# Kernel tuning notes

Hardware: AMD Instinct MI355X
Metric: run time of the kernel (lower is better)

## Reference

```python
import jax, jax.numpy as jnp
import numpy as np

N = 100000
E = 1600000
F_IN, F_HID, F_OUT = 128, 64, 1


def setup_inputs() -> dict:
    key = jax.random.key(0)
    ks = jax.random.split(key, 8)
    x = jax.random.normal(ks[0], (N, F_IN), dtype=jnp.float32)
    edge_index = jax.random.randint(ks[1], (2, E), 0, N, dtype=jnp.int64)
    def glorot(k, fan_in, fan_out):
        scale = jnp.sqrt(2.0 / (fan_in + fan_out)).astype(jnp.float32)
        return jax.random.normal(k, (fan_in, fan_out), dtype=jnp.float32) * scale
    W1 = glorot(ks[2], F_IN, F_HID); b1 = jnp.zeros((F_HID,), jnp.float32)
    W2 = glorot(ks[3], F_HID, F_HID); b2 = jnp.zeros((F_HID,), jnp.float32)
    W3 = glorot(ks[4], F_HID, F_OUT); b3 = jnp.zeros((F_OUT,), jnp.float32)
    return {"x": x, "W1": W1, "b1": b1, "W2": W2, "b2": b2, "W3": W3, "b3": b3, "edge_index": edge_index}


def _gcn_norm(edge_index, n):
    # add self-loops, symmetric D^{-1/2} (A+I) D^{-1/2} normalization (PyG GCNConv default)
    loop = jnp.arange(n, dtype=edge_index.dtype)
    src = jnp.concatenate([edge_index[0], loop])
    dst = jnp.concatenate([edge_index[1], loop])
    deg = jax.ops.segment_sum(jnp.ones_like(src, dtype=jnp.float32), dst, num_segments=n)
    dis = jnp.where(deg > 0, jax.lax.rsqrt(jnp.maximum(deg, 1.0)), 0.0)
    norm = dis[src] * dis[dst]  # [E+N]
    return src, dst, norm


def _gcn_conv(h, W, b, src, dst, norm, n):
    h = h @ W                                   # [N, f_out]
    msg = h[src] * norm[:, None]                # gather + scale, [E+N, f_out]
    out = jax.ops.segment_sum(msg, dst, num_segments=n)  # scatter-add
    return out + b


def reference(x, W1, b1, W2, b2, W3, b3, edge_index):
    n = x.shape[0]
    src, dst, norm = _gcn_norm(edge_index, n)
    h = jax.nn.relu(_gcn_conv(x, W1, b1, src, dst, norm, n))
    h = jax.nn.relu(_gcn_conv(h, W2, b2, src, dst, norm, n))
    h = _gcn_conv(h, W3, b3, src, dst, norm, n)
    return jax.nn.sigmoid(h)
```

## Files before the change

kernel.cpp:

```cpp
#include <hip/hip_runtime.h>
#include <math.h>

#define NN 100000
#define NE 1600000
#define NSHARD 4
#define SHARD_W (NN / NSHARD)
#define NCHUNK 64
#define CHUNK_E (NE / NCHUNK)
#define CHUNK_I4 (CHUNK_E / 4)

typedef __attribute__((ext_vector_type(8))) short bf16x8;
typedef __attribute__((ext_vector_type(4))) float f32x4;
typedef __attribute__((ext_vector_type(2))) float f32x2;

__device__ inline unsigned f2bf(float f) {
    unsigned u = __float_as_uint(f);
    u += 0x7FFFu + ((u >> 16) & 1u);
    return u >> 16;
}
__device__ inline float bflo(unsigned v) { return __uint_as_float(v << 16); }
__device__ inline float bfhi(unsigned v) { return __uint_as_float(v & 0xFFFF0000u); }
__device__ inline f32x2 bfpair(unsigned u) {
    f32x2 r;
    r.x = __uint_as_float(u << 16);
    r.y = __uint_as_float(u & 0xFFFF0000u);
    return r;
}

__global__ __launch_bounds__(256) void k_cnt(const int4* __restrict__ dst4,
                                             unsigned char* __restrict__ cnt,
                                             unsigned char* __restrict__ lrank) {
    __shared__ __align__(16) unsigned ldeg[SHARD_W];
    int t = threadIdx.x;
    int shard = blockIdx.x & (NSHARD - 1);
    int b = blockIdx.x >> 2;
    int lo = shard * SHARD_W;
    uint4 z4 = make_uint4(0u, 0u, 0u, 0u);
    for (int i = t; i < SHARD_W / 4; i += 256) ((uint4*)ldeg)[i] = z4;
    __syncthreads();
    const int4* p = dst4 + b * CHUNK_I4;
    unsigned char* lr = lrank + b * CHUNK_E;
#pragma unroll 4
    for (int j = t; j < CHUNK_I4; j += 256) {
        int4 d = p[j];
        unsigned ex = (unsigned)(d.x - lo);
        unsigned ey = (unsigned)(d.y - lo);
        unsigned ez = (unsigned)(d.z - lo);
        unsigned ew = (unsigned)(d.w - lo);
        if (ex < SHARD_W) lr[4 * j + 0] = (unsigned char)atomicAdd(&ldeg[ex], 1u);
        if (ey < SHARD_W) lr[4 * j + 1] = (unsigned char)atomicAdd(&ldeg[ey], 1u);
        if (ez < SHARD_W) lr[4 * j + 2] = (unsigned char)atomicAdd(&ldeg[ez], 1u);
        if (ew < SHARD_W) lr[4 * j + 3] = (unsigned char)atomicAdd(&ldeg[ew], 1u);
    }
    __syncthreads();
    unsigned* cb32 = (unsigned*)cnt + b * (NN / 4) + shard * (SHARD_W / 4);
    for (int i = t; i < SHARD_W / 4; i += 256) {
        uint4 v = *(const uint4*)&ldeg[4 * i];
        cb32[i] = (v.x & 255u) | ((v.y & 255u) << 8) | ((v.z & 255u) << 16)
                | ((v.w & 255u) << 24);
    }
}

__global__ __launch_bounds__(256) void k_blkscan(unsigned* __restrict__ cnt32,
                                                 int4* __restrict__ deg4) {
    int i = blockIdx.x * 256 + threadIdx.x;
    if (i >= NN / 4) return;
    unsigned c[NCHUNK];
#pragma unroll
    for (int b = 0; b < NCHUNK; ++b) c[b] = cnt32[b * (NN / 4) + i];
    unsigned a0 = 0, a1 = 0, a2 = 0, a3 = 0;
#pragma unroll
    for (int b = 0; b < NCHUNK; ++b) {
        unsigned v = c[b];
        cnt32[b * (NN / 4) + i] = a0 | (a1 << 8) | (a2 << 16) | (a3 << 24);
        a0 += v & 255u;
        a1 += (v >> 8) & 255u;
        a2 += (v >> 16) & 255u;
        a3 += v >> 24;
    }
    deg4[i] = make_int4((int)a0, (int)a1, (int)a2, (int)a3);
}

__global__ void k_bsum(const int* __restrict__ deg, int* __restrict__ bsums) {
    __shared__ int s[256];
    int t = threadIdx.x;
    int i = blockIdx.x * 256 + t;
    s[t] = (i < NN) ? deg[i] : 0;
    __syncthreads();
    for (int off = 128; off > 0; off >>= 1) {
        if (t < off) s[t] += s[t + off];
        __syncthreads();
    }
    if (t == 0) bsums[blockIdx.x] = s[0];
}

__global__ void k_scan512(const int* __restrict__ bsums, int* __restrict__ bscan) {
    __shared__ int s[512];
    int t = threadIdx.x;
    int v = (t < 391) ? bsums[t] : 0;
    s[t] = v;
    __syncthreads();
    for (int off = 1; off < 512; off <<= 1) {
        int x = (t >= off) ? s[t - off] : 0;
        __syncthreads();
        s[t] += x;
        __syncthreads();
    }
    bscan[t] = s[t] - v;
}

__global__ void k_rowptr(const int* __restrict__ deg, const int* __restrict__ bscan,
                         int* __restrict__ rowptr, float* __restrict__ dis) {
    __shared__ int s[256];
    int t = threadIdx.x;
    int i = blockIdx.x * 256 + t;
    int d = (i < NN) ? deg[i] : 0;
    s[t] = d;
    __syncthreads();
    for (int off = 1; off < 256; off <<= 1) {
        int x = (t >= off) ? s[t - off] : 0;
        __syncthreads();
        s[t] += x;
        __syncthreads();
    }
    if (i < NN) {
        int rp = bscan[blockIdx.x] + s[t] - d;
        rowptr[i] = rp;
        dis[i] = rsqrtf((float)(d + 1));
    }
    if (i == 0) rowptr[NN] = NE;
}

__global__ __launch_bounds__(256) void k_build_csr(
    const int4* __restrict__ src4, const int4* __restrict__ dst4,
    const unsigned char* __restrict__ blkoff, const unsigned* __restrict__ lr4,
    const int* __restrict__ rowptr, int* __restrict__ csr) {
    int shard = blockIdx.x & (NSHARD - 1);
    int bsh = blockIdx.x >> 2;
    int stride = (gridDim.x >> 2) * 256;
    int lo = shard * SHARD_W;
    const int NE4 = NE / 4;
    for (int i = bsh * 256 + threadIdx.x; i < NE4; i += stride) {
        int4 d = dst4[i];
        int4 s = src4[i];
        unsigned lr = lr4[i];
        const unsigned char* off = blkoff + (i / CHUNK_I4) * NN;
        unsigned ex = (unsigned)(d.x - lo);
        unsigned ey = (unsigned)(d.y - lo);
        unsigned ez = (unsigned)(d.z - lo);
        unsigned ew = (unsigned)(d.w - lo);
        if (ex < SHARD_W) csr[rowptr[d.x] + off[d.x] + (lr & 255u)] = s.x;
        if (ey < SHARD_W) csr[rowptr[d.y] + off[d.y] + ((lr >> 8) & 255u)] = s.y;
        if (ez < SHARD_W) csr[rowptr[d.z] + off[d.z] + ((lr >> 16) & 255u)] = s.z;
        if (ew < SHARD_W) csr[rowptr[d.w] + off[d.w] + (lr >> 24)] = s.w;
    }
}

#define XS_LD 136
__global__ __launch_bounds__(256) void k_gemm1(
    const float* __restrict__ x, const float* __restrict__ W,
    const float* __restrict__ dis, unsigned short* __restrict__ tsb) {
    __shared__ unsigned short xs[64 * XS_LD];
    __shared__ unsigned short wt[64 * XS_LD];
    int t = threadIdx.x;
    int row0 = blockIdx.x * 64;
    for (int i = t; i < 64 * 64; i += 256) {
        int n = i & 63, k2 = i >> 6;
        float w0 = W[(2 * k2) * 64 + n];
        float w1 = W[(2 * k2 + 1) * 64 + n];
        *(unsigned*)&wt[n * XS_LD + 2 * k2] = f2bf(w0) | (f2bf(w1) << 16);
    }
    for (int i = t; i < 64 * 32; i += 256) {
        int r = i >> 5, c4 = i & 31;
        int gr = row0 + r;
        uint2 p = {0u, 0u};
        if (gr < NN) {
            float4 v = *(const float4*)&x[gr * 128 + 4 * c4];
            p.x = f2bf(v.x) | (f2bf(v.y) << 16);
            p.y = f2bf(v.z) | (f2bf(v.w) << 16);
        }
        *(uint2*)&xs[r * XS_LD + 4 * c4] = p;
    }
    __syncthreads();
    int w = t >> 6, l = t & 63;
    int lm = l & 15, lg = l >> 4;
    const unsigned short* ap = &xs[(16 * w + lm) * XS_LD + 8 * lg];
    const unsigned short* bp = &wt[lm * XS_LD + 8 * lg];
    f32x4 acc0 = {0, 0, 0, 0}, acc1 = {0, 0, 0, 0}, acc2 = {0, 0, 0, 0}, acc3 = {0, 0, 0, 0};
#pragma unroll
    for (int kb = 0; kb < 4; ++kb) {
        bf16x8 a  = *(const bf16x8*)(ap + 32 * kb);
        bf16x8 b0 = *(const bf16x8*)(bp + 32 * kb);
        bf16x8 b1 = *(const bf16x8*)(bp + 16 * XS_LD + 32 * kb);
        bf16x8 b2 = *(const bf16x8*)(bp + 32 * XS_LD + 32 * kb);
        bf16x8 b3 = *(const bf16x8*)(bp + 48 * XS_LD + 32 * kb);
        acc0 = __builtin_amdgcn_mfma_f32_16x16x32_bf16(a, b0, acc0, 0, 0, 0);
        acc1 = __builtin_amdgcn_mfma_f32_16x16x32_bf16(a, b1, acc1, 0, 0, 0);
        acc2 = __builtin_amdgcn_mfma_f32_16x16x32_bf16(a, b2, acc2, 0, 0, 0);
        acc3 = __builtin_amdgcn_mfma_f32_16x16x32_bf16(a, b3, acc3, 0, 0, 0);
    }
    int rbase = row0 + 16 * w + 4 * lg;
#pragma unroll
    for (int r = 0; r < 4; ++r) {
        int row = rbase + r;
        if (row < NN) {
            float dv = dis[row];
            unsigned short* o = &tsb[row * 64 + lm];
            o[0]  = (unsigned short)f2bf(acc0[r] * dv);
            o[16] = (unsigned short)f2bf(acc1[r] * dv);
            o[32] = (unsigned short)f2bf(acc2[r] * dv);
            o[48] = (unsigned short)f2bf(acc3[r] * dv);
        }
    }
}

#define HS_LD 72
__global__ __launch_bounds__(256) void k_gemm2(
    const unsigned short* __restrict__ hb, const float* __restrict__ W,
    const float* __restrict__ dis, unsigned short* __restrict__ tsb) {
    __shared__ unsigned short hs[64 * HS_LD];
    __shared__ unsigned short wh[64 * HS_LD];
    __shared__ unsigned short wl[64 * HS_LD];
    int t = threadIdx.x;
    int row0 = blockIdx.x * 64;
    for (int i = t; i < 64 * 32; i += 256) {
        int n = i & 63, k2 = i >> 6;
        float w0 = W[(2 * k2) * 64 + n];
        float w1 = W[(2 * k2 + 1) * 64 + n];
        unsigned h0 = f2bf(w0), h1 = f2bf(w1);
        *(unsigned*)&wh[n * HS_LD + 2 * k2] = h0 | (h1 << 16);
        float r0 = w0 - bflo(h0), r1 = w1 - bflo(h1);
        *(unsigned*)&wl[n * HS_LD + 2 * k2] = f2bf(r0) | (f2bf(r1) << 16);
    }
    const uint4* h4 = (const uint4*)hb;
    for (int i = t; i < 64 * 8; i += 256) {
        int r = i >> 3, c8 = i & 7;
        int gr = row0 + r;
        uint4 v = (gr < NN) ? h4[gr * 8 + c8] : make_uint4(0u, 0u, 0u, 0u);
        *(uint4*)&hs[r * HS_LD + 8 * c8] = v;
    }
    __syncthreads();
    int w = t >> 6, l = t & 63;
    int lm = l & 15, lg = l >> 4;
    const unsigned short* ap = &hs[(16 * w + lm) * HS_LD + 8 * lg];
    const unsigned short* bh = &wh[lm * HS_LD + 8 * lg];
    const unsigned short* bl = &wl[lm * HS_LD + 8 * lg];
    f32x4 acc0 = {0, 0, 0, 0}, acc1 = {0, 0, 0, 0}, acc2 = {0, 0, 0, 0}, acc3 = {0, 0, 0, 0};
#pragma unroll
    for (int kb = 0; kb < 2; ++kb) {
        bf16x8 a  = *(const bf16x8*)(ap + 32 * kb);
        bf16x8 h0 = *(const bf16x8*)(bh + 32 * kb);
        bf16x8 h1 = *(const bf16x8*)(bh + 16 * HS_LD + 32 * kb);
        bf16x8 h2 = *(const bf16x8*)(bh + 32 * HS_LD + 32 * kb);
        bf16x8 h3 = *(const bf16x8*)(bh + 48 * HS_LD + 32 * kb);
        bf16x8 l0 = *(const bf16x8*)(bl + 32 * kb);
        bf16x8 l1 = *(const bf16x8*)(bl + 16 * HS_LD + 32 * kb);
        bf16x8 l2 = *(const bf16x8*)(bl + 32 * HS_LD + 32 * kb);
        bf16x8 l3 = *(const bf16x8*)(bl + 48 * HS_LD + 32 * kb);
        acc0 = __builtin_amdgcn_mfma_f32_16x16x32_bf16(a, h0, acc0, 0, 0, 0);
        acc1 = __builtin_amdgcn_mfma_f32_16x16x32_bf16(a, h1, acc1, 0, 0, 0);
        acc2 = __builtin_amdgcn_mfma_f32_16x16x32_bf16(a, h2, acc2, 0, 0, 0);
        acc3 = __builtin_amdgcn_mfma_f32_16x16x32_bf16(a, h3, acc3, 0, 0, 0);
        acc0 = __builtin_amdgcn_mfma_f32_16x16x32_bf16(a, l0, acc0, 0, 0, 0);
        acc1 = __builtin_amdgcn_mfma_f32_16x16x32_bf16(a, l1, acc1, 0, 0, 0);
        acc2 = __builtin_amdgcn_mfma_f32_16x16x32_bf16(a, l2, acc2, 0, 0, 0);
        acc3 = __builtin_amdgcn_mfma_f32_16x16x32_bf16(a, l3, acc3, 0, 0, 0);
    }
    int rbase = row0 + 16 * w + 4 * lg;
#pragma unroll
    for (int r = 0; r < 4; ++r) {
        int row = rbase + r;
        if (row < NN) {
            float dv = dis[row];
            unsigned short* o = &tsb[row * 64 + lm];
            o[0]  = (unsigned short)f2bf(acc0[r] * dv);
            o[16] = (unsigned short)f2bf(acc1[r] * dv);
            o[32] = (unsigned short)f2bf(acc2[r] * dv);
            o[48] = (unsigned short)f2bf(acc3[r] * dv);
        }
    }
}

#define AGG_BLOCKS 2048
__global__ __launch_bounds__(256) void k_agg_relu(
    const unsigned short* __restrict__ tsb, const int* __restrict__ rowptr,
    const int* __restrict__ csr, const float* __restrict__ dis,
    const float* __restrict__ b, unsigned short* __restrict__ hb) {
    int wid = blockIdx.x * 4 + (threadIdx.x >> 6);
    const int nwaves = AGG_BLOCKS * 4;
    int lane = threadIdx.x & 63;
    int oct = lane >> 3;
    int fl = lane & 7;
    const uint4* ts128 = (const uint4*)tsb;
    for (int node = wid; node < NN; node += nwaves) {
        f32x2 a0 = {0.f, 0.f}, a1 = {0.f, 0.f}, a2 = {0.f, 0.f}, a3 = {0.f, 0.f};
        if (oct == 0) {
            uint4 v = ts128[node * 8 + fl];
            a0 += bfpair(v.x); a1 += bfpair(v.y); a2 += bfpair(v.z); a3 += bfpair(v.w);
        }
        int e = rowptr[node] + oct, end = rowptr[node + 1];
        for (; e + 8 < end; e += 16) {
            int s0 = csr[e];
            int s1 = csr[e + 8];
            uint4 v0 = ts128[s0 * 8 + fl];
            uint4 v1 = ts128[s1 * 8 + fl];
            a0 += bfpair(v0.x); a1 += bfpair(v0.y); a2 += bfpair(v0.z); a3 += bfpair(v0.w);
            a0 += bfpair(v1.x); a1 += bfpair(v1.y); a2 += bfpair(v1.z); a3 += bfpair(v1.w);
        }
        if (e < end) {
            uint4 v = ts128[csr[e] * 8 + fl];
            a0 += bfpair(v.x); a1 += bfpair(v.y); a2 += bfpair(v.z); a3 += bfpair(v.w);
        }
#pragma unroll
        for (int off = 8; off <= 32; off <<= 1) {
            a0.x += __shfl_xor(a0.x, off); a0.y += __shfl_xor(a0.y, off);
            a1.x += __shfl_xor(a1.x, off); a1.y += __shfl_xor(a1.y, off);
            a2.x += __shfl_xor(a2.x, off); a2.y += __shfl_xor(a2.y, off);
            a3.x += __shfl_xor(a3.x, off); a3.y += __shfl_xor(a3.y, off);
        }
        if (oct == 0) {
            float dv = dis[node];
            float v0 = fmaxf(a0.x * dv + b[8 * fl + 0], 0.f);
            float v1 = fmaxf(a0.y * dv + b[8 * fl + 1], 0.f);
            float v2 = fmaxf(a1.x * dv + b[8 * fl + 2], 0.f);
            float v3 = fmaxf(a1.y * dv + b[8 * fl + 3], 0.f);
            float v4 = fmaxf(a2.x * dv + b[8 * fl + 4], 0.f);
            float v5 = fmaxf(a2.y * dv + b[8 * fl + 5], 0.f);
            float v6 = fmaxf(a3.x * dv + b[8 * fl + 6], 0.f);
            float v7 = fmaxf(a3.y * dv + b[8 * fl + 7], 0.f);
            uint4 p;
            p.x = f2bf(v0) | (f2bf(v1) << 16);
            p.y = f2bf(v2) | (f2bf(v3) << 16);
            p.z = f2bf(v4) | (f2bf(v5) << 16);
            p.w = f2bf(v6) | (f2bf(v7) << 16);
            ((uint4*)hb)[node * 8 + fl] = p;
        }
    }
}

__global__ void k_gemm3(const unsigned short* __restrict__ hb, const float* __restrict__ W3,
                        const float* __restrict__ dis, float* __restrict__ t3) {
    __shared__ float Ws[64];
    if (threadIdx.x < 64) Ws[threadIdx.x] = W3[threadIdx.x];
    __syncthreads();
    int row = blockIdx.x * 256 + threadIdx.x;
    if (row >= NN) return;
    const uint4* hp = (const uint4*)(hb + row * 64);
    float acc = 0.f;
#pragma unroll
    for (int k = 0; k < 8; ++k) {
        uint4 v = hp[k];
        acc += bflo(v.x) * Ws[8 * k + 0] + bfhi(v.x) * Ws[8 * k + 1]
             + bflo(v.y) * Ws[8 * k + 2] + bfhi(v.y) * Ws[8 * k + 3]
             + bflo(v.z) * Ws[8 * k + 4] + bfhi(v.z) * Ws[8 * k + 5]
             + bflo(v.w) * Ws[8 * k + 6] + bfhi(v.w) * Ws[8 * k + 7];
    }
    t3[row] = acc * dis[row];
}

__global__ void k_out(const float* __restrict__ t3, const int* __restrict__ rowptr,
                      const int* __restrict__ csr, const float* __restrict__ dis,
                      const float* __restrict__ b3, float* __restrict__ out) {
    int i = blockIdx.x * 256 + threadIdx.x;
    if (i >= NN) return;
    float acc = t3[i];
    float acc1 = 0.f, acc2 = 0.f, acc3 = 0.f;
    int e = rowptr[i], end = rowptr[i + 1];
    for (; e + 4 <= end; e += 4) {
        acc += t3[csr[e]];
        acc1 += t3[csr[e + 1]];
        acc2 += t3[csr[e + 2]];
        acc3 += t3[csr[e + 3]];
    }
    for (; e < end; ++e) acc += t3[csr[e]];
    float z = ((acc + acc1) + (acc2 + acc3)) * dis[i] + b3[0];
    out[i] = 1.f / (1.f + __expf(-z));
}

extern "C" void kernel_launch(void* const* d_in, const int* in_sizes, int n_in,
                              void* d_out, int out_size, void* d_ws, size_t ws_size,
                              hipStream_t stream) {
    const float* x  = (const float*)d_in[0];
    const float* W1 = (const float*)d_in[1];
    const float* b1 = (const float*)d_in[2];
    const float* W2 = (const float*)d_in[3];
    const float* b2 = (const float*)d_in[4];
    const float* W3 = (const float*)d_in[5];
    const float* b3 = (const float*)d_in[6];
    const int*   ei = (const int*)d_in[7];
    const int* src = ei;
    const int* dst = ei + NE;
    float* out = (float*)d_out;

    unsigned short* TSB = (unsigned short*)d_ws;
    unsigned short* HB  = TSB + (size_t)NN * 64;
    float* dis    = (float*)(HB + (size_t)NN * 64);
    float* t3     = dis + NN;
    int*   deg    = (int*)(t3 + NN);
    int*   rowptr = deg + NN;
    int*   bsums  = rowptr + NN + 8;
    int*   bscan  = bsums + 512;
    int*   csr    = bscan + 512;
    unsigned char* lrank = (unsigned char*)TSB;
    unsigned char* cnt   = (unsigned char*)HB;

    const int nbN = (NN + 255) / 256;
    const int nbG = (NN + 63) / 64;

    k_cnt<<<NSHARD * NCHUNK, 256, 0, stream>>>((const int4*)dst, cnt, lrank);
    k_blkscan<<<(NN / 4 + 255) / 256, 256, 0, stream>>>((unsigned*)cnt, (int4*)deg);
    k_bsum<<<nbN, 256, 0, stream>>>(deg, bsums);
    k_scan512<<<1, 512, 0, stream>>>(bsums, bscan);
    k_rowptr<<<nbN, 256, 0, stream>>>(deg, bscan, rowptr, dis);
    k_build_csr<<<2048, 256, 0, stream>>>((const int4*)src, (const int4*)dst,
                                          cnt, (const unsigned*)lrank, rowptr, csr);

    k_gemm1<<<nbG, 256, 0, stream>>>(x, W1, dis, TSB);
    k_agg_relu<<<AGG_BLOCKS, 256, 0, stream>>>(TSB, rowptr, csr, dis, b1, HB);

    k_gemm2<<<nbG, 256, 0, stream>>>(HB, W2, dis, TSB);
    k_agg_relu<<<AGG_BLOCKS, 256, 0, stream>>>(TSB, rowptr, csr, dis, b2, HB);

    k_gemm3<<<nbN, 256, 0, stream>>>(HB, W3, dis, t3);
    k_out<<<nbN, 256, 0, stream>>>(t3, rowptr, csr, dis, b3, out);
}
```

Before: 290.7 us.

## Fuse degree scan with block sums and process two nodes per wave in aggregation

Merges the per-node chunk-count prefix scan and the per-block degree reduction into one kernel, removing a launch and a re-read of the degree array, though each thread now reads bytes instead of packed 32-bit words. In the aggregation kernel each wavefront now handles two nodes at once, 32 lanes each, with four edge slots per node and four independent gathers in flight per iteration. The shuffle reduction is shortened to match. This is meant to cut idle lanes on low-degree nodes (average degree about 16) and to raise memory-level parallelism, at the cost of more branch divergence between the two halves.

```diff
diff --git a/kernel.cpp b/kernel.cpp
--- a/kernel.cpp
+++ b/kernel.cpp
@@ -61,37 +61,30 @@
     }
 }
 
-__global__ __launch_bounds__(256) void k_blkscan(unsigned* __restrict__ cnt32,
-                                                 int4* __restrict__ deg4) {
+__global__ __launch_bounds__(256) void k_blkscan(unsigned char* __restrict__ cnt,
+                                                 int* __restrict__ deg,
+                                                 int* __restrict__ bsums) {
+    __shared__ int s[256];
     int i = blockIdx.x * 256 + threadIdx.x;
-    if (i >= NN / 4) return;
-    unsigned c[NCHUNK];
-#pragma unroll
-    for (int b = 0; b < NCHUNK; ++b) c[b] = cnt32[b * (NN / 4) + i];
-    unsigned a0 = 0, a1 = 0, a2 = 0, a3 = 0;
-#pragma unroll
-    for (int b = 0; b < NCHUNK; ++b) {
-        unsigned v = c[b];
-        cnt32[b * (NN / 4) + i] = a0 | (a1 << 8) | (a2 << 16) | (a3 << 24);
-        a0 += v & 255u;
-        a1 += (v >> 8) & 255u;
-        a2 += (v >> 16) & 255u;
-        a3 += v >> 24;
-    }
-    deg4[i] = make_int4((int)a0, (int)a1, (int)a2, (int)a3);
-}
-
-__global__ void k_bsum(const int* __restrict__ deg, int* __restrict__ bsums) {
-    __shared__ int s[256];
-    int t = threadIdx.x;
-    int i = blockIdx.x * 256 + t;
-    s[t] = (i < NN) ? deg[i] : 0;
+    int total = 0;
+    if (i < NN) {
+        unsigned a = 0;
+#pragma unroll
+        for (int b = 0; b < NCHUNK; ++b) {
+            unsigned v = cnt[b * NN + i];
+            cnt[b * NN + i] = (unsigned char)a;
+            a += v;
+        }
+        deg[i] = (int)a;
+        total = (int)a;
+    }
+    s[threadIdx.x] = total;
     __syncthreads();
     for (int off = 128; off > 0; off >>= 1) {
-        if (t < off) s[t] += s[t + off];
+        if (threadIdx.x < off) s[threadIdx.x] += s[threadIdx.x + off];
         __syncthreads();
     }
-    if (t == 0) bsums[blockIdx.x] = s[0];
+    if (threadIdx.x == 0) bsums[blockIdx.x] = s[0];
 }
 
 __global__ void k_scan512(const int* __restrict__ bsums, int* __restrict__ bscan) {
@@ -289,36 +282,47 @@
     int wid = blockIdx.x * 4 + (threadIdx.x >> 6);
     const int nwaves = AGG_BLOCKS * 4;
     int lane = threadIdx.x & 63;
-    int oct = lane >> 3;
+    int half = lane >> 5;
+    int oct = (lane >> 3) & 3;
     int fl = lane & 7;
     const uint4* ts128 = (const uint4*)tsb;
-    for (int node = wid; node < NN; node += nwaves) {
+    for (int base = wid * 2; base < NN; base += nwaves * 2) {
+        int node = base + half;
+        bool valid = node < NN;
         f32x2 a0 = {0.f, 0.f}, a1 = {0.f, 0.f}, a2 = {0.f, 0.f}, a3 = {0.f, 0.f};
-        if (oct == 0) {
-            uint4 v = ts128[node * 8 + fl];
-            a0 += bfpair(v.x); a1 += bfpair(v.y); a2 += bfpair(v.z); a3 += bfpair(v.w);
-        }
-        int e = rowptr[node] + oct, end = rowptr[node + 1];
-        for (; e + 8 < end; e += 16) {
-            int s0 = csr[e];
-            int s1 = csr[e + 8];
-            uint4 v0 = ts128[s0 * 8 + fl];
-            uint4 v1 = ts128[s1 * 8 + fl];
-            a0 += bfpair(v0.x); a1 += bfpair(v0.y); a2 += bfpair(v0.z); a3 += bfpair(v0.w);
-            a0 += bfpair(v1.x); a1 += bfpair(v1.y); a2 += bfpair(v1.z); a3 += bfpair(v1.w);
-        }
-        if (e < end) {
-            uint4 v = ts128[csr[e] * 8 + fl];
-            a0 += bfpair(v.x); a1 += bfpair(v.y); a2 += bfpair(v.z); a3 += bfpair(v.w);
-        }
-#pragma unroll
-        for (int off = 8; off <= 32; off <<= 1) {
+        if (valid) {
+            if (oct == 0) {
+                uint4 v = ts128[node * 8 + fl];
+                a0 += bfpair(v.x); a1 += bfpair(v.y); a2 += bfpair(v.z); a3 += bfpair(v.w);
+            }
+            int e = rowptr[node] + oct, end = rowptr[node + 1];
+            for (; e + 12 < end; e += 16) {
+                int s0 = csr[e];
+                int s1 = csr[e + 4];
+                int s2 = csr[e + 8];
+                int s3 = csr[e + 12];
+                uint4 v0 = ts128[s0 * 8 + fl];
+                uint4 v1 = ts128[s1 * 8 + fl];
+                uint4 v2 = ts128[s2 * 8 + fl];
+                uint4 v3 = ts128[s3 * 8 + fl];
+                a0 += bfpair(v0.x); a1 += bfpair(v0.y); a2 += bfpair(v0.z); a3 += bfpair(v0.w);
+                a0 += bfpair(v1.x); a1 += bfpair(v1.y); a2 += bfpair(v1.z); a3 += bfpair(v1.w);
+                a0 += bfpair(v2.x); a1 += bfpair(v2.y); a2 += bfpair(v2.z); a3 += bfpair(v2.w);
+                a0 += bfpair(v3.x); a1 += bfpair(v3.y); a2 += bfpair(v3.z); a3 += bfpair(v3.w);
+            }
+            for (; e < end; e += 4) {
+                uint4 v = ts128[csr[e] * 8 + fl];
+                a0 += bfpair(v.x); a1 += bfpair(v.y); a2 += bfpair(v.z); a3 += bfpair(v.w);
+            }
+        }
+#pragma unroll
+        for (int off = 8; off <= 16; off <<= 1) {
             a0.x += __shfl_xor(a0.x, off); a0.y += __shfl_xor(a0.y, off);
             a1.x += __shfl_xor(a1.x, off); a1.y += __shfl_xor(a1.y, off);
             a2.x += __shfl_xor(a2.x, off); a2.y += __shfl_xor(a2.y, off);
             a3.x += __shfl_xor(a3.x, off); a3.y += __shfl_xor(a3.y, off);
         }
-        if (oct == 0) {
+        if (valid && oct == 0) {
             float dv = dis[node];
             float v0 = fmaxf(a0.x * dv + b[8 * fl + 0], 0.f);
             float v1 = fmaxf(a0.y * dv + b[8 * fl + 1], 0.f);
@@ -408,8 +412,7 @@
     const int nbG = (NN + 63) / 64;
 
     k_cnt<<<NSHARD * NCHUNK, 256, 0, stream>>>((const int4*)dst, cnt, lrank);
-    k_blkscan<<<(NN / 4 + 255) / 256, 256, 0, stream>>>((unsigned*)cnt, (int4*)deg);
-    k_bsum<<<nbN, 256, 0, stream>>>(deg, bsums);
+    k_blkscan<<<nbN, 256, 0, stream>>>(cnt, deg, bsums);
     k_scan512<<<1, 512, 0, stream>>>(bsums, bscan);
     k_rowptr<<<nbN, 256, 0, stream>>>(deg, bscan, rowptr, dis);
     k_build_csr<<<2048, 256, 0, stream>>>((const int4*)src, (const int4*)dst,
```

Result: faster. 273.2 us (-6.0%).
